# Optimization experiments

Measured on AMD Instinct MI355X. Metric: run time of the kernel, lower is better.

## Reference

```python
import jax, jax.numpy as jnp
import numpy as np

D_MODEL = 1024
NHEAD = 16
HEAD_DIM = D_MODEL // NHEAD
NPOS_MAX = 1000
SEQ = 1024
BATCH = 4


def setup_inputs() -> dict:
    key = jax.random.key(0)
    ks = jax.random.split(key, 10)
    s = 0.02
    return {
        "x": jax.random.normal(ks[0], (SEQ, BATCH, D_MODEL), dtype=jnp.float32),
        "Wq": jax.random.normal(ks[1], (D_MODEL, D_MODEL), dtype=jnp.float32) * s,
        "bq": jnp.zeros((D_MODEL,), dtype=jnp.float32),
        "Wk": jax.random.normal(ks[2], (D_MODEL, D_MODEL), dtype=jnp.float32) * s,
        "bk": jnp.zeros((D_MODEL,), dtype=jnp.float32),
        "Wv": jax.random.normal(ks[3], (D_MODEL, D_MODEL), dtype=jnp.float32) * s,
        "bv": jnp.zeros((D_MODEL,), dtype=jnp.float32),
        "Wo": jax.random.normal(ks[4], (D_MODEL, D_MODEL), dtype=jnp.float32) * s,
        "bo": jnp.zeros((D_MODEL,), dtype=jnp.float32),
        "pos_emb": jax.random.normal(ks[5], (1, HEAD_DIM, NPOS_MAX), dtype=jnp.float32) * s,
    }


def _cope(query, attn_logits, pos_emb):
    # query: (H,B,S,D); attn_logits: (H,B,S,S); pos_emb: (1,D,npos)
    gates = jax.nn.sigmoid(attn_logits)
    # reverse cumulative sum along the key axis
    pos = jnp.cumsum(gates[..., ::-1], axis=-1)[..., ::-1]
    pos = jnp.minimum(pos, NPOS_MAX - 1)
    pos_ceil = jnp.ceil(pos).astype(jnp.int32)
    pos_floor = jnp.floor(pos).astype(jnp.int32)
    # (H,B,S,npos): interpolation logits for every integer position
    logits_int = jnp.einsum("hbsd,dn->hbsn", query, pos_emb[0])
    logits_ceil = jnp.take_along_axis(logits_int, pos_ceil, axis=-1)
    logits_floor = jnp.take_along_axis(logits_int, pos_floor, axis=-1)
    w = pos - pos_floor.astype(pos.dtype)
    return logits_ceil * w + logits_floor * (1.0 - w)


def reference(x, Wq, bq, Wk, bk, Wv, bv, Wo, bo, pos_emb):
    S, B, _ = x.shape
    # torch Linear: x @ W.T + b; weights here are already (in,out) so x @ W + b
    def split_heads(t):
        # (S,B,d_model) -> (H,B,S,D)  (matches .view(S,B,H,D).transpose(0,2))
        return t.reshape(S, B, NHEAD, HEAD_DIM).transpose(2, 1, 0, 3)

    q = split_heads(x @ Wq + bq)
    k = split_heads(x @ Wk + bk)
    v = split_heads(x @ Wv + bv)

    scale = 1.0 / (HEAD_DIM ** 0.5)
    attn_logits = jnp.einsum("hbsd,hbtd->hbst", q, k) * scale
    attn_logits = attn_logits + _cope(q, attn_logits, pos_emb)
    attn = jax.nn.softmax(attn_logits, axis=-1)
    out = jnp.einsum("hbst,hbtd->hbsd", attn, v)
    # (H,B,S,D) -> (S,B,d_model)
    out = out.transpose(2, 1, 0, 3).reshape(S, B, D_MODEL)
    return out @ Wo + bo
```

## Files before the change

kernel.cpp:

```cpp
#include <hip/hip_runtime.h>
#include <hip/hip_bf16.h>

#define D_MODEL 1024
#define NHEAD 16
#define HEAD_DIM 64
#define SEQ 1024
#define BATCH 4

typedef unsigned short us;
typedef __attribute__((ext_vector_type(8))) short short8;
typedef __attribute__((ext_vector_type(4))) float f32x4;

#define MFMA16 __builtin_amdgcn_mfma_f32_16x16x32_bf16

__device__ __forceinline__ float sigmoidf_(float x) {
  return 1.0f / (1.0f + __expf(-x));
}
__device__ __forceinline__ us f2bf(float x) {
  union { float f; unsigned u; } v; v.f = x;
  unsigned r = v.u + 0x7fffu + ((v.u >> 16) & 1u);
  return (us)(r >> 16);
}
__device__ __forceinline__ float bf2f(us s) {
  union { unsigned u; float f; } v; v.u = ((unsigned)s) << 16; return v.f;
}
__device__ __forceinline__ void split_bf(float v, us& h, us& l) {
  h = f2bf(v);
  l = f2bf(v - bf2f(h));
}
__device__ __forceinline__ void async16(us* lds, const us* g) {
  __builtin_amdgcn_global_load_lds(
      (const __attribute__((address_space(1))) unsigned int*)(const void*)g,
      (__attribute__((address_space(3))) unsigned int*)(void*)lds, 16, 0, 0);
}

__global__ __launch_bounds__(256) void prep_k(
    const float* __restrict__ x, const float* __restrict__ Wq,
    const float* __restrict__ Wk, const float* __restrict__ Wv,
    const float* __restrict__ Wo, const float* __restrict__ pe,
    us* __restrict__ xh, us* __restrict__ xl, us* __restrict__ wqk,
    us* __restrict__ wvh, us* __restrict__ wvl, us* __restrict__ woh,
    us* __restrict__ wol, us* __restrict__ pet)
{
  __shared__ float tile[32][33];
  const int bid = blockIdx.x, tid = threadIdx.x;
  if (bid < 2048) {
    int i0 = bid * 2048 + tid * 8;
    float4 v0 = *(const float4*)(x + i0);
    float4 v1 = *(const float4*)(x + i0 + 4);
    float vv[8] = {v0.x, v0.y, v0.z, v0.w, v1.x, v1.y, v1.z, v1.w};
    short8 hh, ll;
    #pragma unroll
    for (int j = 0; j < 8; ++j) {
      us h, l; split_bf(vv[j], h, l);
      hh[j] = (short)h; ll[j] = (short)l;
    }
    *(short8*)(xh + i0) = hh;
    *(short8*)(xl + i0) = ll;
  } else if (bid < 6144) {
    int wj = bid - 2048;
    int w = wj >> 10, t = wj & 1023;
    int k0 = (t >> 5) * 32, n0 = (t & 31) * 32;
    const float* W = (w == 0) ? Wq : (w == 1) ? Wk : (w == 2) ? Wv : Wo;
    int tx = tid & 31, ty = tid >> 5;
    #pragma unroll
    for (int rep = 0; rep < 4; ++rep) {
      int ky = ty * 4 + rep;
      tile[ky][tx] = W[(size_t)(k0 + ky) * 1024 + n0 + tx];
    }
    __syncthreads();
    #pragma unroll
    for (int rep = 0; rep < 4; ++rep) {
      int ny = ty * 4 + rep;
      float v = tile[tx][ny];
      int n = n0 + ny, k = k0 + tx;
      if (w < 2) {
        wqk[(size_t)(w * 1024 + n) * 1024 + k] = f2bf(v);
      } else {
        us h, l; split_bf(v, h, l);
        us* dh = (w == 2) ? wvh : woh;
        us* dl = (w == 2) ? wvl : wol;
        dh[(size_t)n * 1024 + k] = h;
        dl[(size_t)n * 1024 + k] = l;
      }
    }
  } else {
    int pj = bid - 6144;
    int k0 = (pj & 1) * 32, n0 = (pj >> 1) * 32;
    int tx = tid & 31, ty = tid >> 5;
    #pragma unroll
    for (int rep = 0; rep < 4; ++rep) {
      int ky = ty * 4 + rep;
      tile[ky][tx] = (n0 + tx < 1000) ? pe[(size_t)(k0 + ky) * 1000 + n0 + tx] : 0.f;
    }
    __syncthreads();
    #pragma unroll
    for (int rep = 0; rep < 4; ++rep) {
      int ny = ty * 4 + rep;
      int n = n0 + ny;
      if (n < 1000) pet[(size_t)n * 64 + k0 + tx] = f2bf(tile[tx][ny]);
    }
  }
}

template<int TERMS, int TN>
__global__ __launch_bounds__(256) void mgemm(
    const us* __restrict__ A0, const us* __restrict__ A1,
    const us* __restrict__ B0, const us* __restrict__ B1,
    const float* __restrict__ bias0, const float* __restrict__ bias1,
    void* out0, void* out1, int mode)
{
  constexpr int PA = (TERMS == 3) ? 2 : 1;
  constexpr int NJ = TN / 32;
  constexpr int NW = TN / 2;
  __shared__ us As[PA][128][32];
  __shared__ us Bs[PA][TN][32];
  const int tid = threadIdx.x, ln = tid & 63, wv = tid >> 6;
  const int col = ln & 15, quad = ln >> 4;
  const int wr = wv >> 1, wc = wv & 1;
  const int m0 = blockIdx.y * 128, n0 = blockIdx.x * TN;
  const us* Ap[2] = {A0, A1};
  const us* Bp[2] = {B0, B1};

  f32x4 acc[4][NJ];
  #pragma unroll
  for (int i = 0; i < 4; ++i)
    #pragma unroll
    for (int j = 0; j < NJ; ++j) acc[i][j] = (f32x4){0.f, 0.f, 0.f, 0.f};

  for (int kt = 0; kt < 1024; kt += 32) {
    #pragma unroll
    for (int p = 0; p < PA; ++p)
      #pragma unroll
      for (int j = 0; j < 2; ++j) {
        int c = j * 256 + wv * 64 + ln;
        int m = c >> 2;
        int kq = (c & 3) ^ ((c >> 3) & 3);
        async16((us*)&As[p][0][0] + (size_t)(j * 256 + wv * 64) * 8,
                Ap[p] + (size_t)(m0 + m) * 1024 + kt + kq * 8);
      }
    #pragma unroll
    for (int p = 0; p < PA; ++p)
      #pragma unroll
      for (int j = 0; j < TN / 64; ++j) {
        int c = j * 256 + wv * 64 + ln;
        int n = c >> 2;
        int kq = (c & 3) ^ ((c >> 3) & 3);
        async16((us*)&Bs[p][0][0] + (size_t)(j * 256 + wv * 64) * 8,
                Bp[p] + (size_t)(n0 + n) * 1024 + kt + kq * 8);
      }
    __syncthreads();

    short8 a0[4], a1[4], b0[NJ], b1[NJ];
    #pragma unroll
    for (int i = 0; i < 4; ++i) {
      int r = wr * 64 + i * 16 + col;
      int q = quad ^ ((r >> 1) & 3);
      a0[i] = *(const short8*)&As[0][r][q * 8];
      if constexpr (TERMS == 3) a1[i] = *(const short8*)&As[1][r][q * 8];
    }
    #pragma unroll
    for (int j = 0; j < NJ; ++j) {
      int r = wc * NW + j * 16 + col;
      int q = quad ^ ((r >> 1) & 3);
      b0[j] = *(const short8*)&Bs[0][r][q * 8];
      if constexpr (TERMS == 3) b1[j] = *(const short8*)&Bs[1][r][q * 8];
    }
    #pragma unroll
    for (int i = 0; i < 4; ++i)
      #pragma unroll
      for (int j = 0; j < NJ; ++j) {
        acc[i][j] = MFMA16(a0[i], b0[j], acc[i][j], 0, 0, 0);
        if constexpr (TERMS == 3) {
          acc[i][j] = MFMA16(a0[i], b1[j], acc[i][j], 0, 0, 0);
          acc[i][j] = MFMA16(a1[i], b0[j], acc[i][j], 0, 0, 0);
        }
      }
    __syncthreads();
  }

  #pragma unroll
  for (int i = 0; i < 4; ++i)
    #pragma unroll
    for (int j = 0; j < NJ; ++j)
      #pragma unroll
      for (int r = 0; r < 4; ++r) {
        int grow = m0 + wr * 64 + i * 16 + quad * 4 + r;
        int gcol = n0 + wc * NW + j * 16 + col;
        float val = acc[i][j][r];
        if (mode == 0) {
          val += (gcol < 1024 ? bias0 : bias1)[gcol & 1023];
          int h = (gcol >> 6) & 15, d = gcol & 63, b = grow & 3, s = grow >> 2;
          ((us*)(gcol < 1024 ? out0 : out1))
              [(size_t)((h * 4 + b) * 1024 + s) * 64 + d] = f2bf(val);
        } else if (mode == 1) {
          val += bias0[gcol];
          int h = gcol >> 6, d = gcol & 63, b = grow & 3, s = grow >> 2;
          size_t idx = (size_t)((h * 4 + b) * 64 + d) * 1024 + s;
          ((us*)out0)[idx] = f2bf(val);
        } else {
          val += bias0[gcol];
          ((float*)out0)[(size_t)grow * 1024 + gcol] = val;
        }
      }
}

__global__ __launch_bounds__(1024) void attn_k(
    const us* __restrict__ qb, const us* __restrict__ kb,
    const us* __restrict__ vth, const us* __restrict__ pet,
    us* __restrict__ ah, us* __restrict__ al)
{
  __shared__ us S_s[16][1032];
  __shared__ alignas(16) us li_s[16][1024];
  __shared__ float qinv_s[16];

  const int tid = threadIdx.x;
  const int lane = tid & 63;
  const int wv = tid >> 6;
  const int col = lane & 15;
  const int quad = lane >> 4;
  const int id = blockIdx.x;
  const int hb = ((id >> 3) & 7) * 8 + (id & 7);
  const int s0 = (id >> 6) * 16;

  const us* Q = qb + ((size_t)hb * SEQ + s0) * HEAD_DIM;
  const us* K = kb + (size_t)hb * SEQ * HEAD_DIM;
  const us* Vh = vth + (size_t)hb * HEAD_DIM * SEQ;

  short8 aq0 = *(const short8*)(Q + col * 64 + quad * 8);
  short8 aq1 = *(const short8*)(Q + col * 64 + 32 + quad * 8);

  #pragma unroll
  for (int kt = 0; kt < 4; ++kt) {
    int t0 = wv * 64 + kt * 16;
    const us* Kr = K + (size_t)(t0 + col) * 64;
    short8 b0 = *(const short8*)(Kr + quad * 8);
    short8 b1 = *(const short8*)(Kr + 32 + quad * 8);
    f32x4 sc = {0.f, 0.f, 0.f, 0.f};
    sc = MFMA16(aq0, b0, sc, 0, 0, 0);
    sc = MFMA16(aq1, b1, sc, 0, 0, 0);
    #pragma unroll
    for (int r = 0; r < 4; ++r)
      S_s[quad * 4 + r][t0 + col] = f2bf(sc[r] * 0.125f);
  }

  #pragma unroll
  for (int nt = 0; nt < 4; ++nt) {
    int n = wv * 64 + nt * 16 + col;
    int nn = (n < 1000) ? n : 999;
    short8 b0 = *(const short8*)(pet + (size_t)nn * 64 + quad * 8);
    short8 b1 = *(const short8*)(pet + (size_t)nn * 64 + 32 + quad * 8);
    f32x4 li = {0.f, 0.f, 0.f, 0.f};
    li = MFMA16(aq0, b0, li, 0, 0, 0);
    li = MFMA16(aq1, b1, li, 0, 0, 0);
    #pragma unroll
    for (int r = 0; r < 4; ++r)
      li_s[quad * 4 + r][n] = f2bf(li[r]);
  }
  __syncthreads();

  {
    const int q = wv;
    short8 s8a = *(const short8*)&S_s[q][lane * 16];
    short8 s8b = *(const short8*)&S_s[q][lane * 16 + 8];
    float s[16], suf[16];
    #pragma unroll
    for (int j = 0; j < 8; ++j) s[j] = bf2f((us)s8a[j]);
    #pragma unroll
    for (int j = 0; j < 8; ++j) s[8 + j] = bf2f((us)s8b[j]);
    float run = 0.f;
    #pragma unroll
    for (int j = 15; j >= 0; --j) {
      run += sigmoidf_(s[j]);
      suf[j] = run;
    }
    float v = run;
    #pragma unroll
    for (int off = 1; off < 64; off <<= 1) {
      float u = __shfl_down(v, off);
      v += (lane + off < 64) ? u : 0.f;
    }
    float after = v - run;
    float lg[16];
    float m = -1e30f;
    #pragma unroll
    for (int j = 0; j < 16; ++j) {
      float p = fminf(after + suf[j], 999.0f);
      float fl = floorf(p);
      int fi = (int)fl;
      int ci = (int)ceilf(p);
      float w = p - fl;
      float lf = bf2f(li_s[q][fi]);
      float lc = bf2f(li_s[q][ci]);
      lg[j] = s[j] + lc * w + lf * (1.f - w);
      m = fmaxf(m, lg[j]);
    }
    #pragma unroll
    for (int off = 1; off < 64; off <<= 1) m = fmaxf(m, __shfl_xor(m, off));
    float rs = 0.f;
    short8 p8a, p8b;
    #pragma unroll
    for (int j = 0; j < 8; ++j) {
      float e = __expf(lg[j] - m);
      rs += e;
      p8a[j] = (short)f2bf(e);
    }
    #pragma unroll
    for (int j = 0; j < 8; ++j) {
      float e = __expf(lg[8 + j] - m);
      rs += e;
      p8b[j] = (short)f2bf(e);
    }
    #pragma unroll
    for (int off = 1; off < 64; off <<= 1) rs += __shfl_xor(rs, off);
    *(short8*)&S_s[q][lane * 16] = p8a;
    *(short8*)&S_s[q][lane * 16 + 8] = p8b;
    if (lane == 0) qinv_s[q] = 1.0f / rs;
  }
  __syncthreads();

  const int wk = wv >> 2, wd = wv & 3;
  const int d0 = wd * 16;
  f32x4 o = {0.f, 0.f, 0.f, 0.f};
  #pragma unroll
  for (int kt = 0; kt < 8; ++kt) {
    int t0 = wk * 256 + kt * 32;
    short8 a = *(const short8*)&S_s[col][t0 + quad * 8];
    short8 bh = *(const short8*)(Vh + (size_t)(d0 + col) * 1024 + t0 + quad * 8);
    o = MFMA16(a, bh, o, 0, 0, 0);
  }
  __syncthreads();
  f32x4* red = (f32x4*)&li_s[0][0];
  red[wv * 64 + lane] = o;
  __syncthreads();
  if (wv < 4) {
    f32x4 t0v = red[(0 * 4 + wv) * 64 + lane];
    f32x4 t1v = red[(1 * 4 + wv) * 64 + lane];
    f32x4 t2v = red[(2 * 4 + wv) * 64 + lane];
    f32x4 t3v = red[(3 * 4 + wv) * 64 + lane];
    const int b_ = hb & 3, h = hb >> 2;
    #pragma unroll
    for (int r = 0; r < 4; ++r) {
      int q = quad * 4 + r;
      float val = (t0v[r] + t1v[r] + t2v[r] + t3v[r]) * qinv_s[q];
      size_t idx = (size_t)((s0 + q) * 4 + b_) * 1024 + h * 64 + wv * 16 + col;
      us hh, ll; split_bf(val, hh, ll);
      ah[idx] = hh;
      al[idx] = ll;
    }
  }
}

extern "C" void kernel_launch(void* const* d_in, const int* in_sizes, int n_in,
                              void* d_out, int out_size, void* d_ws, size_t ws_size,
                              hipStream_t stream) {
  const float* x  = (const float*)d_in[0];
  const float* Wq = (const float*)d_in[1];
  const float* bq = (const float*)d_in[2];
  const float* Wk = (const float*)d_in[3];
  const float* bk = (const float*)d_in[4];
  const float* Wv = (const float*)d_in[5];
  const float* bv = (const float*)d_in[6];
  const float* Wo = (const float*)d_in[7];
  const float* bo = (const float*)d_in[8];
  const float* pe = (const float*)d_in[9];

  us* w = (us*)d_ws;
  us* xh  = w;
  us* xl  = w + 4194304;
  us* wqk = w + 8388608;
  us* wvh = w + 10485760;
  us* wvl = w + 11534336;
  us* woh = w + 12582912;
  us* wol = w + 13631488;
  us* pet = w + 14680064;
  us* qb  = w + 14745600;
  us* kb  = w + 18939904;
  us* vth = w + 23134208;
  us* ah  = w + 31522816;
  us* al  = w + 35717120;

  prep_k<<<6208, 256, 0, stream>>>(x, Wq, Wk, Wv, Wo, pe,
                                   xh, xl, wqk, wvh, wvl, woh, wol, pet);
  mgemm<1, 128><<<dim3(16, 32), 256, 0, stream>>>(
      xh, nullptr, wqk, nullptr, bq, bk, qb, kb, 0);
  mgemm<3, 64><<<dim3(16, 32), 256, 0, stream>>>(
      xh, xl, wvh, wvl, bv, bv, vth, nullptr, 1);
  attn_k<<<dim3(4096), 1024, 0, stream>>>(qb, kb, vth, pet, ah, al);
  mgemm<3, 64><<<dim3(16, 32), 256, 0, stream>>>(
      ah, al, woh, wol, bo, bo, (void*)d_out, nullptr, 2);
}
```

Baseline: 403.8 us.

## Switch from split-bf16 three-term GEMMs to single-pass fp16 MFMA everywhere

Replaces bf16 storage and the hi/lo split (three MFMA terms) used for the V and output projections with plain fp16 values and a single fp16 MFMA pass. Every GEMM now uses a 128x128 tile, the extra low-part buffers are dropped, and the attention kernel also runs its MFMAs in fp16. This cuts MFMA work and memory traffic for the V and O projections and the prep conversion. The cost is lower accuracy than the split representation and a risk of fp16 overflow or precision loss, for example in the logits and the unnormalized exp values.

```diff
diff --git a/kernel.cpp b/kernel.cpp
--- a/kernel.cpp
+++ b/kernel.cpp
@@ -9,24 +9,19 @@
 
 typedef unsigned short us;
 typedef __attribute__((ext_vector_type(8))) short short8;
+typedef __attribute__((ext_vector_type(8))) _Float16 half8;
 typedef __attribute__((ext_vector_type(4))) float f32x4;
 
-#define MFMA16 __builtin_amdgcn_mfma_f32_16x16x32_bf16
+#define MFMAH __builtin_amdgcn_mfma_f32_16x16x32_f16
 
 __device__ __forceinline__ float sigmoidf_(float x) {
   return 1.0f / (1.0f + __expf(-x));
 }
-__device__ __forceinline__ us f2bf(float x) {
-  union { float f; unsigned u; } v; v.f = x;
-  unsigned r = v.u + 0x7fffu + ((v.u >> 16) & 1u);
-  return (us)(r >> 16);
-}
-__device__ __forceinline__ float bf2f(us s) {
-  union { unsigned u; float f; } v; v.u = ((unsigned)s) << 16; return v.f;
-}
-__device__ __forceinline__ void split_bf(float v, us& h, us& l) {
-  h = f2bf(v);
-  l = f2bf(v - bf2f(h));
+__device__ __forceinline__ us f2h(float x) {
+  union { _Float16 h; us u; } v; v.h = (_Float16)x; return v.u;
+}
+__device__ __forceinline__ float h2f(us s) {
+  union { _Float16 h; us u; } v; v.u = s; return (float)v.h;
 }
 __device__ __forceinline__ void async16(us* lds, const us* g) {
   __builtin_amdgcn_global_load_lds(
@@ -38,9 +33,8 @@
     const float* __restrict__ x, const float* __restrict__ Wq,
     const float* __restrict__ Wk, const float* __restrict__ Wv,
     const float* __restrict__ Wo, const float* __restrict__ pe,
-    us* __restrict__ xh, us* __restrict__ xl, us* __restrict__ wqk,
-    us* __restrict__ wvh, us* __restrict__ wvl, us* __restrict__ woh,
-    us* __restrict__ wol, us* __restrict__ pet)
+    us* __restrict__ xh, us* __restrict__ wqk, us* __restrict__ wv,
+    us* __restrict__ wo, us* __restrict__ pet)
 {
   __shared__ float tile[32][33];
   const int bid = blockIdx.x, tid = threadIdx.x;
@@ -49,19 +43,16 @@
     float4 v0 = *(const float4*)(x + i0);
     float4 v1 = *(const float4*)(x + i0 + 4);
     float vv[8] = {v0.x, v0.y, v0.z, v0.w, v1.x, v1.y, v1.z, v1.w};
-    short8 hh, ll;
-    #pragma unroll
-    for (int j = 0; j < 8; ++j) {
-      us h, l; split_bf(vv[j], h, l);
-      hh[j] = (short)h; ll[j] = (short)l;
-    }
+    short8 hh;
+    #pragma unroll
+    for (int j = 0; j < 8; ++j) hh[j] = (short)f2h(vv[j]);
     *(short8*)(xh + i0) = hh;
-    *(short8*)(xl + i0) = ll;
   } else if (bid < 6144) {
     int wj = bid - 2048;
     int w = wj >> 10, t = wj & 1023;
     int k0 = (t >> 5) * 32, n0 = (t & 31) * 32;
     const float* W = (w == 0) ? Wq : (w == 1) ? Wk : (w == 2) ? Wv : Wo;
+    us* dst = (w == 0) ? wqk : (w == 1) ? (wqk + 1048576) : (w == 2) ? wv : wo;
     int tx = tid & 31, ty = tid >> 5;
     #pragma unroll
     for (int rep = 0; rep < 4; ++rep) {
@@ -72,17 +63,8 @@
     #pragma unroll
     for (int rep = 0; rep < 4; ++rep) {
       int ny = ty * 4 + rep;
-      float v = tile[tx][ny];
       int n = n0 + ny, k = k0 + tx;
-      if (w < 2) {
-        wqk[(size_t)(w * 1024 + n) * 1024 + k] = f2bf(v);
-      } else {
-        us h, l; split_bf(v, h, l);
-        us* dh = (w == 2) ? wvh : woh;
-        us* dl = (w == 2) ? wvl : wol;
-        dh[(size_t)n * 1024 + k] = h;
-        dl[(size_t)n * 1024 + k] = l;
-      }
+      dst[(size_t)n * 1024 + k] = f2h(tile[tx][ny]);
     }
   } else {
     int pj = bid - 6144;
@@ -98,106 +80,87 @@
     for (int rep = 0; rep < 4; ++rep) {
       int ny = ty * 4 + rep;
       int n = n0 + ny;
-      if (n < 1000) pet[(size_t)n * 64 + k0 + tx] = f2bf(tile[tx][ny]);
-    }
-  }
-}
-
-template<int TERMS, int TN>
+      if (n < 1000) pet[(size_t)n * 64 + k0 + tx] = f2h(tile[tx][ny]);
+    }
+  }
+}
+
 __global__ __launch_bounds__(256) void mgemm(
-    const us* __restrict__ A0, const us* __restrict__ A1,
-    const us* __restrict__ B0, const us* __restrict__ B1,
+    const us* __restrict__ A0, const us* __restrict__ B0,
     const float* __restrict__ bias0, const float* __restrict__ bias1,
     void* out0, void* out1, int mode)
 {
-  constexpr int PA = (TERMS == 3) ? 2 : 1;
-  constexpr int NJ = TN / 32;
-  constexpr int NW = TN / 2;
-  __shared__ us As[PA][128][32];
-  __shared__ us Bs[PA][TN][32];
+  __shared__ us As[128][32];
+  __shared__ us Bs[128][32];
   const int tid = threadIdx.x, ln = tid & 63, wv = tid >> 6;
   const int col = ln & 15, quad = ln >> 4;
   const int wr = wv >> 1, wc = wv & 1;
-  const int m0 = blockIdx.y * 128, n0 = blockIdx.x * TN;
-  const us* Ap[2] = {A0, A1};
-  const us* Bp[2] = {B0, B1};
-
-  f32x4 acc[4][NJ];
+  const int m0 = blockIdx.y * 128, n0 = blockIdx.x * 128;
+
+  f32x4 acc[4][4];
   #pragma unroll
   for (int i = 0; i < 4; ++i)
     #pragma unroll
-    for (int j = 0; j < NJ; ++j) acc[i][j] = (f32x4){0.f, 0.f, 0.f, 0.f};
+    for (int j = 0; j < 4; ++j) acc[i][j] = (f32x4){0.f, 0.f, 0.f, 0.f};
 
   for (int kt = 0; kt < 1024; kt += 32) {
     #pragma unroll
-    for (int p = 0; p < PA; ++p)
-      #pragma unroll
-      for (int j = 0; j < 2; ++j) {
-        int c = j * 256 + wv * 64 + ln;
-        int m = c >> 2;
-        int kq = (c & 3) ^ ((c >> 3) & 3);
-        async16((us*)&As[p][0][0] + (size_t)(j * 256 + wv * 64) * 8,
-                Ap[p] + (size_t)(m0 + m) * 1024 + kt + kq * 8);
-      }
-    #pragma unroll
-    for (int p = 0; p < PA; ++p)
-      #pragma unroll
-      for (int j = 0; j < TN / 64; ++j) {
-        int c = j * 256 + wv * 64 + ln;
-        int n = c >> 2;
-        int kq = (c & 3) ^ ((c >> 3) & 3);
-        async16((us*)&Bs[p][0][0] + (size_t)(j * 256 + wv * 64) * 8,
-                Bp[p] + (size_t)(n0 + n) * 1024 + kt + kq * 8);
-      }
+    for (int j = 0; j < 2; ++j) {
+      int c = j * 256 + wv * 64 + ln;
+      int m = c >> 2;
+      int kq = (c & 3) ^ ((c >> 3) & 3);
+      async16((us*)&As[0][0] + (size_t)(j * 256 + wv * 64) * 8,
+              A0 + (size_t)(m0 + m) * 1024 + kt + kq * 8);
+    }
+    #pragma unroll
+    for (int j = 0; j < 2; ++j) {
+      int c = j * 256 + wv * 64 + ln;
+      int n = c >> 2;
+      int kq = (c & 3) ^ ((c >> 3) & 3);
+      async16((us*)&Bs[0][0] + (size_t)(j * 256 + wv * 64) * 8,
+              B0 + (size_t)(n0 + n) * 1024 + kt + kq * 8);
+    }
     __syncthreads();
 
-    short8 a0[4], a1[4], b0[NJ], b1[NJ];
+    half8 a0[4], b0[4];
     #pragma unroll
     for (int i = 0; i < 4; ++i) {
       int r = wr * 64 + i * 16 + col;
       int q = quad ^ ((r >> 1) & 3);
-      a0[i] = *(const short8*)&As[0][r][q * 8];
-      if constexpr (TERMS == 3) a1[i] = *(const short8*)&As[1][r][q * 8];
-    }
-    #pragma unroll
-    for (int j = 0; j < NJ; ++j) {
-      int r = wc * NW + j * 16 + col;
+      a0[i] = *(const half8*)&As[r][q * 8];
+    }
+    #pragma unroll
+    for (int j = 0; j < 4; ++j) {
+      int r = wc * 64 + j * 16 + col;
       int q = quad ^ ((r >> 1) & 3);
-      b0[j] = *(const short8*)&Bs[0][r][q * 8];
-      if constexpr (TERMS == 3) b1[j] = *(const short8*)&Bs[1][r][q * 8];
+      b0[j] = *(const half8*)&Bs[r][q * 8];
     }
     #pragma unroll
     for (int i = 0; i < 4; ++i)
       #pragma unroll
-      for (int j = 0; j < NJ; ++j) {
-        acc[i][j] = MFMA16(a0[i], b0[j], acc[i][j], 0, 0, 0);
-        if constexpr (TERMS == 3) {
-          acc[i][j] = MFMA16(a0[i], b1[j], acc[i][j], 0, 0, 0);
-          acc[i][j] = MFMA16(a1[i], b0[j], acc[i][j], 0, 0, 0);
-        }
-      }
+      for (int j = 0; j < 4; ++j)
+        acc[i][j] = MFMAH(a0[i], b0[j], acc[i][j], 0, 0, 0);
     __syncthreads();
   }
 
   #pragma unroll
   for (int i = 0; i < 4; ++i)
     #pragma unroll
-    for (int j = 0; j < NJ; ++j)
+    for (int j = 0; j < 4; ++j)
       #pragma unroll
       for (int r = 0; r < 4; ++r) {
         int grow = m0 + wr * 64 + i * 16 + quad * 4 + r;
-        int gcol = n0 + wc * NW + j * 16 + col;
+        int gcol = n0 + wc * 64 + j * 16 + col;
         float val = acc[i][j][r];
         if (mode == 0) {
           val += (gcol < 1024 ? bias0 : bias1)[gcol & 1023];
           int h = (gcol >> 6) & 15, d = gcol & 63, b = grow & 3, s = grow >> 2;
           ((us*)(gcol < 1024 ? out0 : out1))
-              [(size_t)((h * 4 + b) * 1024 + s) * 64 + d] = f2bf(val);
+              [(size_t)((h * 4 + b) * 1024 + s) * 64 + d] = f2h(val);
         } else if (mode == 1) {
           val += bias0[gcol];
           int h = gcol >> 6, d = gcol & 63, b = grow & 3, s = grow >> 2;
-          size_t idx = (size_t)((h * 4 + b) * 64 + d) * 1024 + s;
-          ((us*)out0)[idx] = f2bf(val);
+          ((us*)out0)[(size_t)((h * 4 + b) * 64 + d) * 1024 + s] = f2h(val);
         } else {
           val += bias0[gcol];
           ((float*)out0)[(size_t)grow * 1024 + gcol] = val;
@@ -208,7 +171,7 @@
 __global__ __launch_bounds__(1024) void attn_k(
     const us* __restrict__ qb, const us* __restrict__ kb,
     const us* __restrict__ vth, const us* __restrict__ pet,
-    us* __restrict__ ah, us* __restrict__ al)
+    us* __restrict__ ah)
 {
   __shared__ us S_s[16][1032];
   __shared__ alignas(16) us li_s[16][1024];
@@ -227,35 +190,35 @@
   const us* K = kb + (size_t)hb * SEQ * HEAD_DIM;
   const us* Vh = vth + (size_t)hb * HEAD_DIM * SEQ;
 
-  short8 aq0 = *(const short8*)(Q + col * 64 + quad * 8);
-  short8 aq1 = *(const short8*)(Q + col * 64 + 32 + quad * 8);
+  half8 aq0 = *(const half8*)(Q + col * 64 + quad * 8);
+  half8 aq1 = *(const half8*)(Q + col * 64 + 32 + quad * 8);
 
   #pragma unroll
   for (int kt = 0; kt < 4; ++kt) {
     int t0 = wv * 64 + kt * 16;
     const us* Kr = K + (size_t)(t0 + col) * 64;
-    short8 b0 = *(const short8*)(Kr + quad * 8);
-    short8 b1 = *(const short8*)(Kr + 32 + quad * 8);
+    half8 b0 = *(const half8*)(Kr + quad * 8);
+    half8 b1 = *(const half8*)(Kr + 32 + quad * 8);
     f32x4 sc = {0.f, 0.f, 0.f, 0.f};
-    sc = MFMA16(aq0, b0, sc, 0, 0, 0);
-    sc = MFMA16(aq1, b1, sc, 0, 0, 0);
+    sc = MFMAH(aq0, b0, sc, 0, 0, 0);
+    sc = MFMAH(aq1, b1, sc, 0, 0, 0);
     #pragma unroll
     for (int r = 0; r < 4; ++r)
-      S_s[quad * 4 + r][t0 + col] = f2bf(sc[r] * 0.125f);
+      S_s[quad * 4 + r][t0 + col] = f2h(sc[r] * 0.125f);
   }
 
   #pragma unroll
   for (int nt = 0; nt < 4; ++nt) {
     int n = wv * 64 + nt * 16 + col;
     int nn = (n < 1000) ? n : 999;
-    short8 b0 = *(const short8*)(pet + (size_t)nn * 64 + quad * 8);
-    short8 b1 = *(const short8*)(pet + (size_t)nn * 64 + 32 + quad * 8);
+    half8 b0 = *(const half8*)(pet + (size_t)nn * 64 + quad * 8);
+    half8 b1 = *(const half8*)(pet + (size_t)nn * 64 + 32 + quad * 8);
     f32x4 li = {0.f, 0.f, 0.f, 0.f};
-    li = MFMA16(aq0, b0, li, 0, 0, 0);
-    li = MFMA16(aq1, b1, li, 0, 0, 0);
+    li = MFMAH(aq0, b0, li, 0, 0, 0);
+    li = MFMAH(aq1, b1, li, 0, 0, 0);
     #pragma unroll
     for (int r = 0; r < 4; ++r)
-      li_s[quad * 4 + r][n] = f2bf(li[r]);
+      li_s[quad * 4 + r][n] = f2h(li[r]);
   }
   __syncthreads();
 
@@ -265,9 +228,9 @@
     short8 s8b = *(const short8*)&S_s[q][lane * 16 + 8];
     float s[16], suf[16];
     #pragma unroll
-    for (int j = 0; j < 8; ++j) s[j] = bf2f((us)s8a[j]);
-    #pragma unroll
-    for (int j = 0; j < 8; ++j) s[8 + j] = bf2f((us)s8b[j]);
+    for (int j = 0; j < 8; ++j) s[j] = h2f((us)s8a[j]);
+    #pragma unroll
+    for (int j = 0; j < 8; ++j) s[8 + j] = h2f((us)s8b[j]);
     float run = 0.f;
     #pragma unroll
     for (int j = 15; j >= 0; --j) {
@@ -290,8 +253,8 @@
       int fi = (int)fl;
       int ci = (int)ceilf(p);
       float w = p - fl;
-      float lf = bf2f(li_s[q][fi]);
-      float lc = bf2f(li_s[q][ci]);
+      float lf = h2f(li_s[q][fi]);
+      float lc = h2f(li_s[q][ci]);
       lg[j] = s[j] + lc * w + lf * (1.f - w);
       m = fmaxf(m, lg[j]);
     }
@@ -303,13 +266,13 @@
     for (int j = 0; j < 8; ++j) {
       float e = __expf(lg[j] - m);
       rs += e;
-      p8a[j] = (short)f2bf(e);
+      p8a[j] = (short)f2h(e);
     }
     #pragma unroll
     for (int j = 0; j < 8; ++j) {
       float e = __expf(lg[8 + j] - m);
       rs += e;
-      p8b[j] = (short)f2bf(e);
+      p8b[j] = (short)f2h(e);
     }
     #pragma unroll
     for (int off = 1; off < 64; off <<= 1) rs += __shfl_xor(rs, off);
@@ -325,9 +288,9 @@
   #pragma unroll
   for (int kt = 0; kt < 8; ++kt) {
     int t0 = wk * 256 + kt * 32;
-    short8 a = *(const short8*)&S_s[col][t0 + quad * 8];
-    short8 bh = *(const short8*)(Vh + (size_t)(d0 + col) * 1024 + t0 + quad * 8);
-    o = MFMA16(a, bh, o, 0, 0, 0);
+    half8 a = *(const half8*)&S_s[col][t0 + quad * 8];
+    half8 bh = *(const half8*)(Vh + (size_t)(d0 + col) * 1024 + t0 + quad * 8);
+    o = MFMAH(a, bh, o, 0, 0, 0);
   }
   __syncthreads();
   f32x4* red = (f32x4*)&li_s[0][0];
@@ -344,9 +307,7 @@
       int q = quad * 4 + r;
       float val = (t0v[r] + t1v[r] + t2v[r] + t3v[r]) * qinv_s[q];
       size_t idx = (size_t)((s0 + q) * 4 + b_) * 1024 + h * 64 + wv * 16 + col;
-      us hh, ll; split_bf(val, hh, ll);
-      ah[idx] = hh;
-      al[idx] = ll;
+      ah[idx] = f2h(val);
     }
   }
 }
@@ -367,26 +328,18 @@
 
   us* w = (us*)d_ws;
   us* xh  = w;
-  us* xl  = w + 4194304;
-  us* wqk = w + 8388608;
-  us* wvh = w + 10485760;
-  us* wvl = w + 11534336;
-  us* woh = w + 12582912;
-  us* wol = w + 13631488;
-  us* pet = w + 14680064;
-  us* qb  = w + 14745600;
-  us* kb  = w + 18939904;
-  us* vth = w + 23134208;
-  us* ah  = w + 31522816;
-  us* al  = w + 35717120;
-
-  prep_k<<<6208, 256, 0, stream>>>(x, Wq, Wk, Wv, Wo, pe,
-                                   xh, xl, wqk, wvh, wvl, woh, wol, pet);
-  mgemm<1, 128><<<dim3(16, 32), 256, 0, stream>>>(
-      xh, nullptr, wqk, nullptr, bq, bk, qb, kb, 0);
-  mgemm<3, 64><<<dim3(16, 32), 256, 0, stream>>>(
-      xh, xl, wvh, wvl, bv, bv, vth, nullptr, 1);
-  attn_k<<<dim3(4096), 1024, 0, stream>>>(qb, kb, vth, pet, ah, al);
-  mgemm<3, 64><<<dim3(16, 32), 256, 0, stream>>>(
-      ah, al, woh, wol, bo, bo, (void*)d_out, nullptr, 2);
-}
+  us* wqk = w + 4194304;
+  us* wv_ = w + 6291456;
+  us* wo_ = w + 7340032;
+  us* pet = w + 8388608;
+  us* qb  = w + 8454144;
+  us* kb  = w + 12648448;
+  us* vth = w + 16842752;
+  us* ah  = w + 21037056;
+
+  prep_k<<<6208, 256, 0, stream>>>(x, Wq, Wk, Wv, Wo, pe, xh, wqk, wv_, wo_, pet);
+  mgemm<<<dim3(16, 32), 256, 0, stream>>>(xh, wqk, bq, bk, qb, kb, 0);
+  mgemm<<<dim3(8, 32), 256, 0, stream>>>(xh, wv_, bv, nullptr, vth, nullptr, 1);
+  attn_k<<<dim3(4096), 1024, 0, stream>>>(qb, kb, vth, pet, ah);
+  mgemm<<<dim3(8, 32), 256, 0, stream>>>(ah, wo_, bo, nullptr, (void*)d_out, nullptr, 2);
+}
```

Result: slower. 469.3 us (+16.2%).
